# Optimization experiments

Hardware: AMD Instinct MI355X
Metric: run time of the kernel (lower is better)

Reference implementation:

```python
import jax, jax.numpy as jnp
import numpy as np

GROUP_SIZE = 128


def setup_inputs() -> dict:
    key = jax.random.key(0)
    k1, k2, k3, k4, k5 = jax.random.split(key, 5)
    N, I, O = 16, 4096, 11008
    Ng = I // GROUP_SIZE  # 32
    x = jax.random.normal(k1, (N, I), dtype=jnp.float16)
    # raw int8 bit patterns, represented as int32 in [0, 256) (== value after & 255)
    weight_q = jax.random.randint(k2, (O, I), 0, 256, dtype=jnp.int32)
    scale = (jax.random.uniform(k3, (O, Ng), dtype=jnp.float32) * 0.01 + 0.001).astype(jnp.float16)
    zero = (jax.random.uniform(k4, (O, Ng), dtype=jnp.float32) * 255.0).astype(jnp.float16)
    bias = (jax.random.normal(k5, (O,), dtype=jnp.float32) * 0.02).astype(jnp.float16)
    return {"x": x, "weight_q": weight_q, "scale": scale, "zero": zero, "bias": bias}


def reference(x, weight_q, scale, zero, bias):
    O, I = weight_q.shape
    G = GROUP_SIZE
    Ng = I // G  # I divisible by G here, so no padding branch
    # (weight_q.int16 & 255).uint8 -> fp16, group-wise dequant
    wq = (weight_q & 255).astype(jnp.float16).reshape(O, Ng, G)
    w_fp = (scale[:, :, None] * (wq - zero[:, :, None])).reshape(O, I)  # (O, I) fp16
    # F.linear(x, w_fp, bias)
    return jnp.dot(x, w_fp.T) + bias
```

## Files before the change

kernel.cpp:

```cpp
#include <hip/hip_runtime.h>
#include <hip/hip_fp16.h>


typedef _Float16 v8hf __attribute__((ext_vector_type(8)));
typedef float v4f __attribute__((ext_vector_type(4)));

#define O_DIM 11008
#define I_DIM 4096
#define NGROUP 32

__global__ __launch_bounds__(256) void qgemm(const float* __restrict__ x,
                                             const int* __restrict__ wq,
                                             const float* __restrict__ scale,
                                             const float* __restrict__ zero,
                                             const float* __restrict__ bias,
                                             float* __restrict__ out) {
    __shared__ float red[4][256];

    const int ot  = blockIdx.x;
    const int tid = threadIdx.x;
    const int w   = tid >> 6;
    const int l   = tid & 63;
    const int col = l & 15;
    const int kb  = l >> 4;
    const int o   = ot * 16 + col;

    const int*   __restrict__ wrow = wq + (size_t)o * I_DIM;
    const float* __restrict__ xrow = x  + (size_t)col * I_DIM;

    v4f acc = {0.f, 0.f, 0.f, 0.f};

#pragma unroll 2
    for (int gi = 0; gi < 8; ++gi) {
        const int g = w * 8 + gi;
        const float s   = scale[o * NGROUP + g];
        const float z   = zero [o * NGROUP + g];
        const float nzs = -z * s;
#pragma unroll
        for (int ks = 0; ks < 4; ++ks) {
            const int i0 = g * 128 + ks * 32 + kb * 8;
            const int4   q0 = *(const int4*)  (wrow + i0);
            const int4   q1 = *(const int4*)  (wrow + i0 + 4);
            const float4 x0 = *(const float4*)(xrow + i0);
            const float4 x1 = *(const float4*)(xrow + i0 + 4);
            v8hf a;
            a[0] = (_Float16)x0.x; a[1] = (_Float16)x0.y;
            a[2] = (_Float16)x0.z; a[3] = (_Float16)x0.w;
            a[4] = (_Float16)x1.x; a[5] = (_Float16)x1.y;
            a[6] = (_Float16)x1.z; a[7] = (_Float16)x1.w;
            v8hf bf;
            bf[0] = (_Float16)((float)(q0.x & 255) * s + nzs);
            bf[1] = (_Float16)((float)(q0.y & 255) * s + nzs);
            bf[2] = (_Float16)((float)(q0.z & 255) * s + nzs);
            bf[3] = (_Float16)((float)(q0.w & 255) * s + nzs);
            bf[4] = (_Float16)((float)(q1.x & 255) * s + nzs);
            bf[5] = (_Float16)((float)(q1.y & 255) * s + nzs);
            bf[6] = (_Float16)((float)(q1.z & 255) * s + nzs);
            bf[7] = (_Float16)((float)(q1.w & 255) * s + nzs);
            acc = __builtin_amdgcn_mfma_f32_16x16x32_f16(a, bf, acc, 0, 0, 0);
        }
    }

    *(v4f*)&red[w][l * 4] = acc;
    __syncthreads();

    const int t   = tid;
    const float sum = red[0][t] + red[1][t] + red[2][t] + red[3][t];
    const int l2  = t >> 2;
    const int r   = t & 3;
    const int row = (l2 >> 4) * 4 + r;
    const int oc  = ot * 16 + (l2 & 15);
    out[(size_t)row * O_DIM + oc] = sum + bias[oc];
}

extern "C" void kernel_launch(void* const* d_in, const int* in_sizes, int n_in,
                              void* d_out, int out_size, void* d_ws, size_t ws_size,
                              hipStream_t stream) {
    const float* x   = (const float*)d_in[0];
    const int*   wqp = (const int*)  d_in[1];
    const float* sc  = (const float*)d_in[2];
    const float* zp  = (const float*)d_in[3];
    const float* bp  = (const float*)d_in[4];
    float* out = (float*)d_out;

    qgemm<<<688, 256, 0, stream>>>(x, wqp, sc, zp, bp, out);
}
```

Baseline: 51.19 us.

## Stage weight tiles through LDS with async double-buffered global_load_lds

Weight rows are no longer read directly from global memory by each lane. They are copied into a double-buffered shared-memory tile with the async global_load_lds builtin, which lets the next K-chunk prefetch while the current one is computed. Rows are XOR-swizzled so the shared-memory reads avoid bank conflicts, and each row load is a coalesced 1KB transaction. The cost is a block-wide barrier and a vmcnt(0) wait every step. Those limit the overlap, and the waits also stall on the x loads.

```diff
diff --git a/kernel.cpp b/kernel.cpp
--- a/kernel.cpp
+++ b/kernel.cpp
@@ -8,6 +8,8 @@
 #define O_DIM 11008
 #define I_DIM 4096
 #define NGROUP 32
+#define KSTEP 256
+#define NSTEP 16
 
 __global__ __launch_bounds__(256) void qgemm(const float* __restrict__ x,
                                              const int* __restrict__ wq,
@@ -15,6 +17,7 @@
                                              const float* __restrict__ zero,
                                              const float* __restrict__ bias,
                                              float* __restrict__ out) {
+    __shared__ int   wtile[2][16][KSTEP];
     __shared__ float red[4][256];
 
     const int ot  = blockIdx.x;
@@ -25,24 +28,57 @@
     const int kb  = l >> 4;
     const int o   = ot * 16 + col;
 
-    const int*   __restrict__ wrow = wq + (size_t)o * I_DIM;
-    const float* __restrict__ xrow = x  + (size_t)col * I_DIM;
+    size_t wbase[4];
+#pragma unroll
+    for (int rr = 0; rr < 4; ++rr) {
+        const int r = w * 4 + rr;
+        wbase[rr] = (size_t)(ot * 16 + r) * I_DIM + ((l ^ (r & 7)) << 2);
+    }
+
+    const float* __restrict__ xrow = x + (size_t)col * I_DIM;
+    const int grp_half = w >> 1;
+    const int kk = w * 64;
 
     v4f acc = {0.f, 0.f, 0.f, 0.f};
 
-#pragma unroll 2
-    for (int gi = 0; gi < 8; ++gi) {
-        const int g = w * 8 + gi;
+#pragma unroll
+    for (int rr = 0; rr < 4; ++rr) {
+        const int r = w * 4 + rr;
+        __builtin_amdgcn_global_load_lds(
+            (const __attribute__((address_space(1))) void*)(wq + wbase[rr]),
+            (__attribute__((address_space(3))) void*)&wtile[0][r][0], 16, 0, 0);
+    }
+    asm volatile("s_waitcnt vmcnt(0)");
+    __syncthreads();
+
+    for (int t = 0; t < NSTEP; ++t) {
+        const int tb = t & 1;
+        if (t + 1 < NSTEP) {
+#pragma unroll
+            for (int rr = 0; rr < 4; ++rr) {
+                const int r = w * 4 + rr;
+                __builtin_amdgcn_global_load_lds(
+                    (const __attribute__((address_space(1))) void*)
+                        (wq + wbase[rr] + (size_t)(t + 1) * KSTEP),
+                    (__attribute__((address_space(3))) void*)&wtile[tb ^ 1][r][0],
+                    16, 0, 0);
+            }
+        }
+
+        const int g = t * 2 + grp_half;
         const float s   = scale[o * NGROUP + g];
         const float z   = zero [o * NGROUP + g];
         const float nzs = -z * s;
+        const char* lrow = (const char*)&wtile[tb][col][0];
+
 #pragma unroll
-        for (int ks = 0; ks < 4; ++ks) {
-            const int i0 = g * 128 + ks * 32 + kb * 8;
-            const int4   q0 = *(const int4*)  (wrow + i0);
-            const int4   q1 = *(const int4*)  (wrow + i0 + 4);
-            const float4 x0 = *(const float4*)(xrow + i0);
-            const float4 x1 = *(const float4*)(xrow + i0 + 4);
+        for (int m = 0; m < 2; ++m) {
+            const int u0 = ((kk + m * 32) >> 2) + kb * 2;
+            const int4 q0 = *(const int4*)(lrow + (((u0    ) ^ (col & 7)) << 4));
+            const int4 q1 = *(const int4*)(lrow + (((u0 + 1) ^ (col & 7)) << 4));
+            const float* xp = xrow + t * KSTEP + kk + m * 32 + kb * 8;
+            const float4 x0 = *(const float4*)(xp);
+            const float4 x1 = *(const float4*)(xp + 4);
             v8hf a;
             a[0] = (_Float16)x0.x; a[1] = (_Float16)x0.y;
             a[2] = (_Float16)x0.z; a[3] = (_Float16)x0.w;
@@ -59,15 +95,18 @@
             bf[7] = (_Float16)((float)(q1.w & 255) * s + nzs);
             acc = __builtin_amdgcn_mfma_f32_16x16x32_f16(a, bf, acc, 0, 0, 0);
         }
+
+        asm volatile("s_waitcnt vmcnt(0)");
+        __syncthreads();
     }
 
     *(v4f*)&red[w][l * 4] = acc;
     __syncthreads();
 
-    const int t   = tid;
-    const float sum = red[0][t] + red[1][t] + red[2][t] + red[3][t];
-    const int l2  = t >> 2;
-    const int r   = t & 3;
+    const int t2  = tid;
+    const float sum = red[0][t2] + red[1][t2] + red[2][t2] + red[3][t2];
+    const int l2  = t2 >> 2;
+    const int r   = t2 & 3;
     const int row = (l2 >> 4) * 4 + r;
     const int oc  = ot * 16 + (l2 & 15);
     out[(size_t)row * O_DIM + oc] = sum + bias[oc];
```

Measured after the change: 57.35 us. 1.12x slower.

## Split K across 8 waves, preload activations into registers, nontemporal weight loads

Applied to the files above, without the earlier changes.

The block grows to 8 waves, each covering a 512-wide K slice. Each wave loads and converts its slice of x to fp16 registers up front, and the scale and zero values are read before the MFMA loop. Weight loads become nontemporal 16-byte loads, and the loop is fully unrolled so more weight loads are in flight, to better hide memory latency on this bandwidth-bound int32 weight stream. The cost is heavier register use (16 v8hf of activations) and a larger 8-way shared-memory reduction.

```diff
diff --git a/kernel.cpp b/kernel.cpp
--- a/kernel.cpp
+++ b/kernel.cpp
@@ -3,19 +3,20 @@
 
 
 typedef _Float16 v8hf __attribute__((ext_vector_type(8)));
-typedef float v4f __attribute__((ext_vector_type(4)));
+typedef float    v4f  __attribute__((ext_vector_type(4)));
+typedef int      v4i  __attribute__((ext_vector_type(4)));
 
 #define O_DIM 11008
 #define I_DIM 4096
 #define NGROUP 32
 
-__global__ __launch_bounds__(256) void qgemm(const float* __restrict__ x,
+__global__ __launch_bounds__(512) void qgemm(const float* __restrict__ x,
                                              const int* __restrict__ wq,
                                              const float* __restrict__ scale,
                                              const float* __restrict__ zero,
                                              const float* __restrict__ bias,
                                              float* __restrict__ out) {
-    __shared__ float red[4][256];
+    __shared__ float red[8][256];
 
     const int ot  = blockIdx.x;
     const int tid = threadIdx.x;
@@ -24,53 +25,65 @@
     const int col = l & 15;
     const int kb  = l >> 4;
     const int o   = ot * 16 + col;
+    const int k0  = w * 512;
 
-    const int*   __restrict__ wrow = wq + (size_t)o * I_DIM;
-    const float* __restrict__ xrow = x  + (size_t)col * I_DIM;
+    v8hf a_reg[16];
+#pragma unroll
+    for (int i = 0; i < 16; ++i) {
+        const float* xp = x + (size_t)col * I_DIM + k0 + i * 32 + kb * 8;
+        const float4 x0 = *(const float4*)(xp);
+        const float4 x1 = *(const float4*)(xp + 4);
+        a_reg[i][0] = (_Float16)x0.x; a_reg[i][1] = (_Float16)x0.y;
+        a_reg[i][2] = (_Float16)x0.z; a_reg[i][3] = (_Float16)x0.w;
+        a_reg[i][4] = (_Float16)x1.x; a_reg[i][5] = (_Float16)x1.y;
+        a_reg[i][6] = (_Float16)x1.z; a_reg[i][7] = (_Float16)x1.w;
+    }
+    float s_[4], nzs_[4];
+#pragma unroll
+    for (int gi = 0; gi < 4; ++gi) {
+        const int g = w * 4 + gi;
+        const float s = scale[o * NGROUP + g];
+        const float z = zero [o * NGROUP + g];
+        s_[gi] = s; nzs_[gi] = -z * s;
+    }
 
+    const int* __restrict__ wrow = wq + (size_t)o * I_DIM;
     v4f acc = {0.f, 0.f, 0.f, 0.f};
 
-#pragma unroll 2
-    for (int gi = 0; gi < 8; ++gi) {
-        const int g = w * 8 + gi;
-        const float s   = scale[o * NGROUP + g];
-        const float z   = zero [o * NGROUP + g];
-        const float nzs = -z * s;
+#pragma unroll
+    for (int gi = 0; gi < 4; ++gi) {
+        const float s = s_[gi], nzs = nzs_[gi];
 #pragma unroll
         for (int ks = 0; ks < 4; ++ks) {
-            const int i0 = g * 128 + ks * 32 + kb * 8;
-            const int4   q0 = *(const int4*)  (wrow + i0);
-            const int4   q1 = *(const int4*)  (wrow + i0 + 4);
-            const float4 x0 = *(const float4*)(xrow + i0);
-            const float4 x1 = *(const float4*)(xrow + i0 + 4);
-            v8hf a;
-            a[0] = (_Float16)x0.x; a[1] = (_Float16)x0.y;
-            a[2] = (_Float16)x0.z; a[3] = (_Float16)x0.w;
-            a[4] = (_Float16)x1.x; a[5] = (_Float16)x1.y;
-            a[6] = (_Float16)x1.z; a[7] = (_Float16)x1.w;
+            const int i0 = k0 + gi * 128 + ks * 32 + kb * 8;
+            const v4i q0 = __builtin_nontemporal_load((const v4i*)(wrow + i0));
+            const v4i q1 = __builtin_nontemporal_load((const v4i*)(wrow + i0) + 1);
             v8hf bf;
-            bf[0] = (_Float16)((float)(q0.x & 255) * s + nzs);
-            bf[1] = (_Float16)((float)(q0.y & 255) * s + nzs);
-            bf[2] = (_Float16)((float)(q0.z & 255) * s + nzs);
-            bf[3] = (_Float16)((float)(q0.w & 255) * s + nzs);
-            bf[4] = (_Float16)((float)(q1.x & 255) * s + nzs);
-            bf[5] = (_Float16)((float)(q1.y & 255) * s + nzs);
-            bf[6] = (_Float16)((float)(q1.z & 255) * s + nzs);
-            bf[7] = (_Float16)((float)(q1.w & 255) * s + nzs);
-            acc = __builtin_amdgcn_mfma_f32_16x16x32_f16(a, bf, acc, 0, 0, 0);
+            bf[0] = (_Float16)((float)(q0[0] & 255) * s + nzs);
+            bf[1] = (_Float16)((float)(q0[1] & 255) * s + nzs);
+            bf[2] = (_Float16)((float)(q0[2] & 255) * s + nzs);
+            bf[3] = (_Float16)((float)(q0[3] & 255) * s + nzs);
+            bf[4] = (_Float16)((float)(q1[0] & 255) * s + nzs);
+            bf[5] = (_Float16)((float)(q1[1] & 255) * s + nzs);
+            bf[6] = (_Float16)((float)(q1[2] & 255) * s + nzs);
+            bf[7] = (_Float16)((float)(q1[3] & 255) * s + nzs);
+            acc = __builtin_amdgcn_mfma_f32_16x16x32_f16(a_reg[gi * 4 + ks], bf,
+                                                         acc, 0, 0, 0);
         }
     }
 
     *(v4f*)&red[w][l * 4] = acc;
     __syncthreads();
 
-    const int t   = tid;
-    const float sum = red[0][t] + red[1][t] + red[2][t] + red[3][t];
-    const int l2  = t >> 2;
-    const int r   = t & 3;
-    const int row = (l2 >> 4) * 4 + r;
-    const int oc  = ot * 16 + (l2 & 15);
-    out[(size_t)row * O_DIM + oc] = sum + bias[oc];
+    if (tid < 256) {
+        float sum = red[0][tid] + red[1][tid] + red[2][tid] + red[3][tid]
+                  + red[4][tid] + red[5][tid] + red[6][tid] + red[7][tid];
+        const int l2  = tid >> 2;
+        const int r   = tid & 3;
+        const int row = (l2 >> 4) * 4 + r;
+        const int oc  = ot * 16 + (l2 & 15);
+        out[(size_t)row * O_DIM + oc] = sum + bias[oc];
+    }
 }
 
 extern "C" void kernel_launch(void* const* d_in, const int* in_sizes, int n_in,
@@ -83,5 +96,5 @@
     const float* bp  = (const float*)d_in[4];
     float* out = (float*)d_out;
 
-    qgemm<<<688, 256, 0, stream>>>(x, wqp, sc, zp, bp, out);
+    qgemm<<<688, 512, 0, stream>>>(x, wqp, sc, zp, bp, out);
 }
```

Measured after the change: 59.11 us. 15.5% more time.
